# Performance work log

Hardware: AMD Instinct MI355X
Metric: run time of the kernel (lower is better)

Reference implementation:

```python
import jax, jax.numpy as jnp
import numpy as np

N_NODES = 100000
N_EDGES = 1600000
DIM = 64
L = 5
NUM_GRAPHS = 256
BN_EPS = 1e-5


def setup_inputs() -> dict:
    key = jax.random.key(0)
    ks = jax.random.split(key, 8)
    x = jax.random.normal(ks[0], (N_NODES, DIM), dtype=jnp.float32)
    edge_index = jax.random.randint(ks[1], (2, N_EDGES), 0, N_NODES, dtype=jnp.int32).astype(jnp.int64)
    batch = jnp.sort(jax.random.randint(ks[2], (N_NODES,), 0, NUM_GRAPHS, dtype=jnp.int32)).astype(jnp.int64)
    W1 = jax.random.normal(ks[3], (L, DIM, DIM), dtype=jnp.float32) * (1.0 / np.sqrt(DIM))
    b1 = jnp.zeros((L, DIM), dtype=jnp.float32)
    W2 = jax.random.normal(ks[4], (L, DIM, DIM), dtype=jnp.float32) * (1.0 / np.sqrt(DIM))
    b2 = jnp.zeros((L, DIM), dtype=jnp.float32)
    gamma = jnp.ones((L, DIM), dtype=jnp.float32)
    beta = jnp.zeros((L, DIM), dtype=jnp.float32)
    return {"x": x, "edge_index": edge_index, "batch": batch, "W1": W1, "b1": b1, "W2": W2, "b2": b2, "gamma": gamma, "beta": beta}


def reference(x, edge_index, batch, W1, b1, W2, b2, gamma, beta):
    src, dst = edge_index[0], edge_index[1]
    n = x.shape[0]
    h = x
    xs = []
    for i in range(L):
        # GINConv (eps=0): h_i' = MLP(h_i + sum_{j->i} h_j), scatter-add over edges
        agg = jax.ops.segment_sum(h[src], dst, num_segments=n)
        z = h + agg
        z = jnp.maximum(z @ W1[i] + b1[i], 0.0) @ W2[i] + b2[i]
        z = jnp.maximum(z, 0.0)  # outer ReLU
        # BatchNorm1d, training-mode batch stats (biased var)
        mu = jnp.mean(z, axis=0)
        var = jnp.mean((z - mu) ** 2, axis=0)
        z = (z - mu) * jax.lax.rsqrt(var + BN_EPS) * gamma[i] + beta[i]
        xs.append(z)
        h = z
    counts = jax.ops.segment_sum(jnp.ones((n,), dtype=x.dtype), batch, num_segments=NUM_GRAPHS)
    counts = jnp.maximum(counts, 1.0)[:, None]
    xpool = [jax.ops.segment_sum(z, batch, num_segments=NUM_GRAPHS) / counts for z in xs]
    return jnp.concatenate(xpool, axis=1), jnp.concatenate(xs, axis=1)
```

## Files before the change

kernel.cpp:

```cpp
#include <hip/hip_runtime.h>

#define N_NODES 100000
#define N_EDGES 1600000
#define DIM 64
#define NLAYERS 5
#define NUM_GRAPHS 256
#define BN_EPS 1e-5f
#define STATS_BLOCKS 256
#define CSR_CAP 64
#define OV_CAP 65536

__global__ void build_csr_kernel(const int* __restrict__ ei, int* __restrict__ cursor,
                                 int* __restrict__ csr, int* __restrict__ ovcnt,
                                 int* __restrict__ ovedges) {
    int e = blockIdx.x * 256 + threadIdx.x;
    if (e >= N_EDGES) return;
    int s = ei[e];
    int t = ei[N_EDGES + e];
    int slot = atomicAdd(&cursor[t], 1);
    if (slot < CSR_CAP) {
        csr[(long)t * CSR_CAP + slot] = s;
    } else {
        int o = atomicAdd(ovcnt, 1);
        if (o < OV_CAP) ovedges[o] = e;
    }
}

__global__ void pad_csr_kernel(const int* __restrict__ cursor, int* __restrict__ csr) {
    int n = blockIdx.x * 256 + threadIdx.x;
    if (n >= N_NODES) return;
    int cnt = min(cursor[n], CSR_CAP);
    int cnt8 = (cnt + 7) & ~7;
    for (int k = cnt; k < cnt8; ++k) csr[(long)n * CSR_CAP + k] = 0;
}

__global__ __launch_bounds__(256) void aggregate_kernel(
        const int* __restrict__ csr, const int* __restrict__ deg,
        const float* __restrict__ h, int hstride, float* __restrict__ agg) {
    long tid = (long)blockIdx.x * 256 + threadIdx.x;
    int n = (int)(tid >> 6);
    int d = (int)(tid & 63);
    if (n >= N_NODES) return;
    int cnt = min(deg[n], CSR_CAP);
    int cnt8 = (cnt + 7) & ~7;
    const int* row = csr + (long)n * CSR_CAP;
    float a0 = 0.f, a1 = 0.f, a2 = 0.f, a3 = 0.f;
    float a4 = 0.f, a5 = 0.f, a6 = 0.f, a7 = 0.f;
    for (int k = 0; k < cnt8; k += 8) {
        int s0 = row[k + 0], s1 = row[k + 1], s2 = row[k + 2], s3 = row[k + 3];
        int s4 = row[k + 4], s5 = row[k + 5], s6 = row[k + 6], s7 = row[k + 7];
        float v0 = h[(long)s0 * hstride + d];
        float v1 = h[(long)s1 * hstride + d];
        float v2 = h[(long)s2 * hstride + d];
        float v3 = h[(long)s3 * hstride + d];
        float v4 = h[(long)s4 * hstride + d];
        float v5 = h[(long)s5 * hstride + d];
        float v6 = h[(long)s6 * hstride + d];
        float v7 = h[(long)s7 * hstride + d];
        if (k + 0 < cnt) a0 += v0;
        if (k + 1 < cnt) a1 += v1;
        if (k + 2 < cnt) a2 += v2;
        if (k + 3 < cnt) a3 += v3;
        if (k + 4 < cnt) a4 += v4;
        if (k + 5 < cnt) a5 += v5;
        if (k + 6 < cnt) a6 += v6;
        if (k + 7 < cnt) a7 += v7;
    }
    agg[(long)n * DIM + d] = ((a0 + a1) + (a2 + a3)) + ((a4 + a5) + (a6 + a7));
}

__global__ void overflow_kernel(const int* __restrict__ ovedges, const int* __restrict__ ovcnt,
                                const int* __restrict__ ei, const float* __restrict__ h,
                                int hstride, float* __restrict__ agg) {
    int cnt = *ovcnt;
    if (cnt > OV_CAP) cnt = OV_CAP;
    int w = (blockIdx.x * blockDim.x + threadIdx.x) >> 6;
    int d = threadIdx.x & 63;
    int nw = (gridDim.x * blockDim.x) >> 6;
    for (int i = w; i < cnt; i += nw) {
        int e = ovedges[i];
        int s = ei[e];
        int t = ei[N_EDGES + e];
        atomicAdd(&agg[(long)t * DIM + d], h[(long)s * hstride + d]);
    }
}

__global__ __launch_bounds__(256) void mlp_gemm_kernel(
        const float* __restrict__ in, int in_stride, const float* __restrict__ agg,
        const float* __restrict__ W, const float* __restrict__ b,
        float* __restrict__ out) {
    __shared__ __align__(16) float sW[DIM * DIM];
    __shared__ float sb[DIM];
    for (int k = threadIdx.x; k < DIM * DIM / 4; k += 256)
        ((float4*)sW)[k] = ((const float4*)W)[k];
    if (threadIdx.x < DIM) sb[threadIdx.x] = b[threadIdx.x];
    __syncthreads();

    int n = blockIdx.x * 256 + threadIdx.x;
    if (n >= N_NODES) return;
    const float* inr = in + (long)n * in_stride;
    const float* ar = agg ? agg + (long)n * DIM : nullptr;

    float acc[DIM];
#pragma unroll
    for (int j = 0; j < DIM; ++j) acc[j] = sb[j];

    for (int d4 = 0; d4 < DIM / 4; ++d4) {
        float4 zv = *(const float4*)(inr + d4 * 4);
        if (ar) {
            float4 g = *(const float4*)(ar + d4 * 4);
            zv.x += g.x; zv.y += g.y; zv.z += g.z; zv.w += g.w;
        }
        const float* w0 = sW + (d4 * 4 + 0) * DIM;
        const float* w1 = sW + (d4 * 4 + 1) * DIM;
        const float* w2 = sW + (d4 * 4 + 2) * DIM;
        const float* w3 = sW + (d4 * 4 + 3) * DIM;
#pragma unroll
        for (int j = 0; j < DIM; j += 4) {
            float4 a0 = *(const float4*)(w0 + j);
            float4 a1 = *(const float4*)(w1 + j);
            float4 a2 = *(const float4*)(w2 + j);
            float4 a3 = *(const float4*)(w3 + j);
            acc[j + 0] += zv.x * a0.x + zv.y * a1.x + zv.z * a2.x + zv.w * a3.x;
            acc[j + 1] += zv.x * a0.y + zv.y * a1.y + zv.z * a2.y + zv.w * a3.y;
            acc[j + 2] += zv.x * a0.z + zv.y * a1.z + zv.z * a2.z + zv.w * a3.z;
            acc[j + 3] += zv.x * a0.w + zv.y * a1.w + zv.z * a2.w + zv.w * a3.w;
        }
    }

    float* o = out + (long)n * DIM;
#pragma unroll
    for (int k = 0; k < DIM; k += 4) {
        float4 v = { fmaxf(acc[k + 0], 0.f), fmaxf(acc[k + 1], 0.f),
                     fmaxf(acc[k + 2], 0.f), fmaxf(acc[k + 3], 0.f) };
        *(float4*)(o + k) = v;
    }
}

__global__ void stats_partial_kernel(const float* __restrict__ z, float* __restrict__ partials) {
    __shared__ float red[2 * 256];
    int d = threadIdx.x & 63;
    int slot = threadIdx.x >> 6;
    const int S = STATS_BLOCKS * 4;
    float s1 = 0.f, s2 = 0.f;
    int n = blockIdx.x * 4 + slot;
    for (; n + 3 * S < N_NODES; n += 4 * S) {
        float v0 = z[(long)(n + 0 * S) * DIM + d];
        float v1 = z[(long)(n + 1 * S) * DIM + d];
        float v2 = z[(long)(n + 2 * S) * DIM + d];
        float v3 = z[(long)(n + 3 * S) * DIM + d];
        s1 += v0 + v1 + v2 + v3;
        s2 += v0 * v0 + v1 * v1 + v2 * v2 + v3 * v3;
    }
    for (; n < N_NODES; n += S) {
        float v = z[(long)n * DIM + d];
        s1 += v;
        s2 += v * v;
    }
    red[threadIdx.x] = s1;
    red[256 + threadIdx.x] = s2;
    __syncthreads();
    if (threadIdx.x < 64) {
        float a = red[d] + red[64 + d] + red[128 + d] + red[192 + d];
        float c = red[256 + d] + red[320 + d] + red[384 + d] + red[448 + d];
        partials[blockIdx.x * 128 + d] = a;
        partials[blockIdx.x * 128 + 64 + d] = c;
    }
}

__global__ void stats_finalize_kernel(const float* __restrict__ partials,
                                      const float* __restrict__ gamma,
                                      const float* __restrict__ beta,
                                      float* __restrict__ ss) {
    int d = threadIdx.x;
    if (d >= 64) return;
    float s1 = 0.f, s2 = 0.f;
    for (int b = 0; b < STATS_BLOCKS; ++b) {
        s1 += partials[b * 128 + d];
        s2 += partials[b * 128 + 64 + d];
    }
    float mu = s1 * (1.f / N_NODES);
    float var = s2 * (1.f / N_NODES) - mu * mu;
    float rs = 1.f / sqrtf(fmaxf(var, 0.f) + BN_EPS);
    float sc = gamma[d] * rs;
    ss[d] = sc;
    ss[64 + d] = beta[d] - mu * sc;
}

__global__ void bn_apply_kernel(const float* __restrict__ z, const float* __restrict__ ss,
                                float* __restrict__ outxs) {
    long t = (long)blockIdx.x * 256 + threadIdx.x;
    if (t >= (long)N_NODES * (DIM / 4)) return;
    int r = (int)(t & 15);
    long n = t >> 4;
    float4 v = ((const float4*)(z + n * DIM))[r];
    float4 sc = ((const float4*)ss)[r];
    float4 sh = ((const float4*)(ss + DIM))[r];
    float4 o = { v.x * sc.x + sh.x, v.y * sc.y + sh.y,
                 v.z * sc.z + sh.z, v.w * sc.w + sh.w };
    ((float4*)(outxs + n * (DIM * NLAYERS)))[r] = o;
}

__global__ void graph_starts_kernel(const int* __restrict__ batch, int* __restrict__ starts) {
    int g = threadIdx.x;
    if (g > NUM_GRAPHS) return;
    int lo = 0, hi = N_NODES;
    while (lo < hi) {
        int mid = (lo + hi) >> 1;
        if (batch[mid] < g) lo = mid + 1; else hi = mid;
    }
    starts[g] = lo;
}

__global__ void pool_kernel(const float* __restrict__ xs, const int* __restrict__ starts,
                            float* __restrict__ outpool) {
    int g = blockIdx.x;
    int d = threadIdx.x;
    int s = starts[g], e = starts[g + 1];
    const int LD = DIM * NLAYERS;
    float a0 = 0.f, a1 = 0.f, a2 = 0.f, a3 = 0.f;
    float a4 = 0.f, a5 = 0.f, a6 = 0.f, a7 = 0.f;
    int n = s;
    for (; n + 8 <= e; n += 8) {
        a0 += xs[(long)(n + 0) * LD + d];
        a1 += xs[(long)(n + 1) * LD + d];
        a2 += xs[(long)(n + 2) * LD + d];
        a3 += xs[(long)(n + 3) * LD + d];
        a4 += xs[(long)(n + 4) * LD + d];
        a5 += xs[(long)(n + 5) * LD + d];
        a6 += xs[(long)(n + 6) * LD + d];
        a7 += xs[(long)(n + 7) * LD + d];
    }
    for (; n < e; ++n) a0 += xs[(long)n * LD + d];
    float acc = ((a0 + a1) + (a2 + a3)) + ((a4 + a5) + (a6 + a7));
    outpool[(long)g * LD + d] = acc / fmaxf((float)(e - s), 1.f);
}

static inline size_t rup(size_t x) { return (x + 255) & ~(size_t)255; }

extern "C" void kernel_launch(void* const* d_in, const int* in_sizes, int n_in,
                              void* d_out, int out_size, void* d_ws, size_t ws_size,
                              hipStream_t stream) {
    const float* x     = (const float*)d_in[0];
    const int*   ei    = (const int*)d_in[1];
    const int*   batch = (const int*)d_in[2];
    const float* W1    = (const float*)d_in[3];
    const float* b1    = (const float*)d_in[4];
    const float* W2    = (const float*)d_in[5];
    const float* b2    = (const float*)d_in[6];
    const float* gamma = (const float*)d_in[7];
    const float* beta  = (const float*)d_in[8];

    float* out      = (float*)d_out;
    float* out_pool = out;
    float* out_xs   = out + (size_t)NUM_GRAPHS * DIM * NLAYERS;

    char* w = (char*)d_ws;
    int*   csr      = (int*)w;    w += rup((size_t)N_NODES * CSR_CAP * 4);
    int*   cursor   = (int*)w;    w += rup((size_t)N_NODES * 4);
    int*   ovcnt    = (int*)w;    w += 256;
    int*   ovedges  = (int*)w;    w += rup((size_t)OV_CAP * 4);
    float* agg      = (float*)w;  w += rup((size_t)N_NODES * DIM * 4);
    float* bufB     = (float*)w;  w += rup((size_t)N_NODES * DIM * 4);
    float* partials = (float*)w;  w += rup((size_t)STATS_BLOCKS * 128 * 4);
    float* ss       = (float*)w;  w += 512;
    int*   starts   = (int*)w;    w += rup((size_t)(NUM_GRAPHS + 1) * 4);

    hipMemsetAsync(cursor, 0, (size_t)N_NODES * 4, stream);
    hipMemsetAsync(ovcnt, 0, 4, stream);
    build_csr_kernel<<<(N_EDGES + 255) / 256, 256, 0, stream>>>(ei, cursor, csr, ovcnt, ovedges);
    pad_csr_kernel<<<(N_NODES + 255) / 256, 256, 0, stream>>>(cursor, csr);
    graph_starts_kernel<<<1, 320, 0, stream>>>(batch, starts);

    const float* h = x;
    int hs = DIM;
    for (int l = 0; l < NLAYERS; ++l) {
        aggregate_kernel<<<((long)N_NODES * DIM + 255) / 256, 256, 0, stream>>>(csr, cursor, h, hs, agg);
        overflow_kernel<<<16, 256, 0, stream>>>(ovedges, ovcnt, ei, h, hs, agg);
        mlp_gemm_kernel<<<(N_NODES + 255) / 256, 256, 0, stream>>>(
            h, hs, agg, W1 + (size_t)l * DIM * DIM, b1 + (size_t)l * DIM, bufB);
        mlp_gemm_kernel<<<(N_NODES + 255) / 256, 256, 0, stream>>>(
            bufB, DIM, nullptr, W2 + (size_t)l * DIM * DIM, b2 + (size_t)l * DIM, agg);
        stats_partial_kernel<<<STATS_BLOCKS, 256, 0, stream>>>(agg, partials);
        stats_finalize_kernel<<<1, 64, 0, stream>>>(partials, gamma + (size_t)l * DIM,
                                                    beta + (size_t)l * DIM, ss);
        bn_apply_kernel<<<((long)N_NODES * (DIM / 4) + 255) / 256, 256, 0, stream>>>(
            agg, ss, out_xs + (size_t)l * DIM);
        h = out_xs + (size_t)l * DIM;
        hs = DIM * NLAYERS;
    }

    pool_kernel<<<NUM_GRAPHS, 320, 0, stream>>>(out_xs, starts, out_pool);
}
```

Measured before the change: 966.6 us.

## Fuse two MLP GEMMs with BN stats, shrink CSR cap, inline overflow handling

Merges the two per-layer MLP GEMM kernels and the BatchNorm partial-statistics pass into one kernel that keeps the hidden activations in registers and reduces per-block sums via wave shuffles. This removes the intermediate buffer round trip and two launches per layer. The CSR row capacity is halved to cut index memory and padding. Overflow edges are now stored as (dst,src) pairs and scanned linearly inside the aggregate kernel, which replaces the atomic overflow kernel but could be costly if many nodes exceed the smaller cap. CSR building also processes four edges per thread. Register pressure in the fused MLP (two 64-float accumulators) may reduce occupancy.

After: 1.795 ms. 85.7% more time.

```diff
diff --git a/kernel.cpp b/kernel.cpp
--- a/kernel.cpp
+++ b/kernel.cpp
@@ -6,24 +6,32 @@
 #define NLAYERS 5
 #define NUM_GRAPHS 256
 #define BN_EPS 1e-5f
-#define STATS_BLOCKS 256
-#define CSR_CAP 64
+#define CSR_CAP 32
 #define OV_CAP 65536
-
-__global__ void build_csr_kernel(const int* __restrict__ ei, int* __restrict__ cursor,
-                                 int* __restrict__ csr, int* __restrict__ ovcnt,
-                                 int* __restrict__ ovedges) {
-    int e = blockIdx.x * 256 + threadIdx.x;
-    if (e >= N_EDGES) return;
-    int s = ei[e];
-    int t = ei[N_EDGES + e];
-    int slot = atomicAdd(&cursor[t], 1);
-    if (slot < CSR_CAP) {
-        csr[(long)t * CSR_CAP + slot] = s;
-    } else {
-        int o = atomicAdd(ovcnt, 1);
-        if (o < OV_CAP) ovedges[o] = e;
-    }
+#define NBLK ((N_NODES + 255) / 256)
+
+__global__ __launch_bounds__(256) void build_csr_kernel(
+        const int* __restrict__ ei, int* __restrict__ cursor,
+        int* __restrict__ csr, int* __restrict__ ovcnt, int* __restrict__ ovpairs) {
+    const int Q = N_EDGES / 4;
+    int tid = blockIdx.x * 256 + threadIdx.x;
+    if (tid >= Q) return;
+    int e0 = tid, e1 = tid + Q, e2 = tid + 2 * Q, e3 = tid + 3 * Q;
+    int s0 = ei[e0], s1 = ei[e1], s2 = ei[e2], s3 = ei[e3];
+    int t0 = ei[N_EDGES + e0], t1 = ei[N_EDGES + e1];
+    int t2 = ei[N_EDGES + e2], t3 = ei[N_EDGES + e3];
+    int c0 = atomicAdd(&cursor[t0], 1);
+    int c1 = atomicAdd(&cursor[t1], 1);
+    int c2 = atomicAdd(&cursor[t2], 1);
+    int c3 = atomicAdd(&cursor[t3], 1);
+    if (c0 < CSR_CAP) csr[t0 * CSR_CAP + c0] = s0;
+    else { int o = atomicAdd(ovcnt, 1); if (o < OV_CAP) { ovpairs[2*o] = t0; ovpairs[2*o+1] = s0; } }
+    if (c1 < CSR_CAP) csr[t1 * CSR_CAP + c1] = s1;
+    else { int o = atomicAdd(ovcnt, 1); if (o < OV_CAP) { ovpairs[2*o] = t1; ovpairs[2*o+1] = s1; } }
+    if (c2 < CSR_CAP) csr[t2 * CSR_CAP + c2] = s2;
+    else { int o = atomicAdd(ovcnt, 1); if (o < OV_CAP) { ovpairs[2*o] = t2; ovpairs[2*o+1] = s2; } }
+    if (c3 < CSR_CAP) csr[t3 * CSR_CAP + c3] = s3;
+    else { int o = atomicAdd(ovcnt, 1); if (o < OV_CAP) { ovpairs[2*o] = t3; ovpairs[2*o+1] = s3; } }
 }
 
 __global__ void pad_csr_kernel(const int* __restrict__ cursor, int* __restrict__ csr) {
@@ -31,32 +39,34 @@
     if (n >= N_NODES) return;
     int cnt = min(cursor[n], CSR_CAP);
     int cnt8 = (cnt + 7) & ~7;
-    for (int k = cnt; k < cnt8; ++k) csr[(long)n * CSR_CAP + k] = 0;
+    for (int k = cnt; k < cnt8; ++k) csr[n * CSR_CAP + k] = 0;
 }
 
 __global__ __launch_bounds__(256) void aggregate_kernel(
         const int* __restrict__ csr, const int* __restrict__ deg,
+        const int* __restrict__ ovcnt, const int* __restrict__ ovpairs,
         const float* __restrict__ h, int hstride, float* __restrict__ agg) {
     long tid = (long)blockIdx.x * 256 + threadIdx.x;
     int n = (int)(tid >> 6);
     int d = (int)(tid & 63);
     if (n >= N_NODES) return;
-    int cnt = min(deg[n], CSR_CAP);
+    int dval = deg[n];
+    int cnt = min(dval, CSR_CAP);
     int cnt8 = (cnt + 7) & ~7;
-    const int* row = csr + (long)n * CSR_CAP;
+    const int4* row = (const int4*)(csr + n * CSR_CAP);
     float a0 = 0.f, a1 = 0.f, a2 = 0.f, a3 = 0.f;
     float a4 = 0.f, a5 = 0.f, a6 = 0.f, a7 = 0.f;
     for (int k = 0; k < cnt8; k += 8) {
-        int s0 = row[k + 0], s1 = row[k + 1], s2 = row[k + 2], s3 = row[k + 3];
-        int s4 = row[k + 4], s5 = row[k + 5], s6 = row[k + 6], s7 = row[k + 7];
-        float v0 = h[(long)s0 * hstride + d];
-        float v1 = h[(long)s1 * hstride + d];
-        float v2 = h[(long)s2 * hstride + d];
-        float v3 = h[(long)s3 * hstride + d];
-        float v4 = h[(long)s4 * hstride + d];
-        float v5 = h[(long)s5 * hstride + d];
-        float v6 = h[(long)s6 * hstride + d];
-        float v7 = h[(long)s7 * hstride + d];
+        int4 ra = row[k >> 2];
+        int4 rb = row[(k >> 2) + 1];
+        float v0 = h[(long)ra.x * hstride + d];
+        float v1 = h[(long)ra.y * hstride + d];
+        float v2 = h[(long)ra.z * hstride + d];
+        float v3 = h[(long)ra.w * hstride + d];
+        float v4 = h[(long)rb.x * hstride + d];
+        float v5 = h[(long)rb.y * hstride + d];
+        float v6 = h[(long)rb.z * hstride + d];
+        float v7 = h[(long)rb.w * hstride + d];
         if (k + 0 < cnt) a0 += v0;
         if (k + 1 < cnt) a1 += v1;
         if (k + 2 < cnt) a2 += v2;
@@ -66,105 +76,121 @@
         if (k + 6 < cnt) a6 += v6;
         if (k + 7 < cnt) a7 += v7;
     }
+    if (dval > CSR_CAP) {
+        int m = min(*ovcnt, OV_CAP);
+        for (int i = 0; i < m; ++i) {
+            if (ovpairs[2 * i] == n) a0 += h[(long)ovpairs[2 * i + 1] * hstride + d];
+        }
+    }
     agg[(long)n * DIM + d] = ((a0 + a1) + (a2 + a3)) + ((a4 + a5) + (a6 + a7));
 }
 
-__global__ void overflow_kernel(const int* __restrict__ ovedges, const int* __restrict__ ovcnt,
-                                const int* __restrict__ ei, const float* __restrict__ h,
-                                int hstride, float* __restrict__ agg) {
-    int cnt = *ovcnt;
-    if (cnt > OV_CAP) cnt = OV_CAP;
-    int w = (blockIdx.x * blockDim.x + threadIdx.x) >> 6;
-    int d = threadIdx.x & 63;
-    int nw = (gridDim.x * blockDim.x) >> 6;
-    for (int i = w; i < cnt; i += nw) {
-        int e = ovedges[i];
-        int s = ei[e];
-        int t = ei[N_EDGES + e];
-        atomicAdd(&agg[(long)t * DIM + d], h[(long)s * hstride + d]);
-    }
-}
-
-__global__ __launch_bounds__(256) void mlp_gemm_kernel(
+__global__ __launch_bounds__(256) void mlp_fused_kernel(
         const float* __restrict__ in, int in_stride, const float* __restrict__ agg,
-        const float* __restrict__ W, const float* __restrict__ b,
-        float* __restrict__ out) {
-    __shared__ __align__(16) float sW[DIM * DIM];
-    __shared__ float sb[DIM];
-    for (int k = threadIdx.x; k < DIM * DIM / 4; k += 256)
-        ((float4*)sW)[k] = ((const float4*)W)[k];
-    if (threadIdx.x < DIM) sb[threadIdx.x] = b[threadIdx.x];
+        const float* __restrict__ W1, const float* __restrict__ b1,
+        const float* __restrict__ W2, const float* __restrict__ b2,
+        float* __restrict__ z, float* __restrict__ partials) {
+    __shared__ __align__(16) float sW1[DIM * DIM];
+    __shared__ __align__(16) float sW2[DIM * DIM];
+    __shared__ float sb1[DIM], sb2[DIM];
+    __shared__ float red[4][2][DIM];
+    for (int k = threadIdx.x; k < DIM * DIM / 4; k += 256) {
+        ((float4*)sW1)[k] = ((const float4*)W1)[k];
+        ((float4*)sW2)[k] = ((const float4*)W2)[k];
+    }
+    if (threadIdx.x < DIM) { sb1[threadIdx.x] = b1[threadIdx.x]; sb2[threadIdx.x] = b2[threadIdx.x]; }
     __syncthreads();
 
     int n = blockIdx.x * 256 + threadIdx.x;
-    if (n >= N_NODES) return;
-    const float* inr = in + (long)n * in_stride;
-    const float* ar = agg ? agg + (long)n * DIM : nullptr;
-
-    float acc[DIM];
-#pragma unroll
-    for (int j = 0; j < DIM; ++j) acc[j] = sb[j];
-
-    for (int d4 = 0; d4 < DIM / 4; ++d4) {
-        float4 zv = *(const float4*)(inr + d4 * 4);
-        if (ar) {
-            float4 g = *(const float4*)(ar + d4 * 4);
+    bool valid = n < N_NODES;
+
+    float acc1[DIM];
+    float acc2[DIM];
+#pragma unroll
+    for (int j = 0; j < DIM; ++j) acc1[j] = sb1[j];
+#pragma unroll
+    for (int j = 0; j < DIM; ++j) acc2[j] = valid ? sb2[j] : 0.f;
+
+    if (valid) {
+        const float* inr = in + (long)n * in_stride;
+        const float* ar  = agg + (long)n * DIM;
+        for (int d4 = 0; d4 < DIM / 4; ++d4) {
+            float4 zv = ((const float4*)inr)[d4];
+            float4 g  = ((const float4*)ar)[d4];
             zv.x += g.x; zv.y += g.y; zv.z += g.z; zv.w += g.w;
-        }
-        const float* w0 = sW + (d4 * 4 + 0) * DIM;
-        const float* w1 = sW + (d4 * 4 + 1) * DIM;
-        const float* w2 = sW + (d4 * 4 + 2) * DIM;
-        const float* w3 = sW + (d4 * 4 + 3) * DIM;
+            const float* w0 = sW1 + (d4 * 4 + 0) * DIM;
+            const float* w1 = sW1 + (d4 * 4 + 1) * DIM;
+            const float* w2 = sW1 + (d4 * 4 + 2) * DIM;
+            const float* w3 = sW1 + (d4 * 4 + 3) * DIM;
+#pragma unroll
+            for (int j = 0; j < DIM; j += 4) {
+                float4 a0 = *(const float4*)(w0 + j);
+                float4 a1 = *(const float4*)(w1 + j);
+                float4 a2 = *(const float4*)(w2 + j);
+                float4 a3 = *(const float4*)(w3 + j);
+                acc1[j + 0] += zv.x * a0.x + zv.y * a1.x + zv.z * a2.x + zv.w * a3.x;
+                acc1[j + 1] += zv.x * a0.y + zv.y * a1.y + zv.z * a2.y + zv.w * a3.y;
+                acc1[j + 2] += zv.x * a0.z + zv.y * a1.z + zv.z * a2.z + zv.w * a3.z;
+                acc1[j + 3] += zv.x * a0.w + zv.y * a1.w + zv.z * a2.w + zv.w * a3.w;
+            }
+        }
+#pragma unroll
+        for (int k4 = 0; k4 < DIM / 4; ++k4) {
+            float h0 = fmaxf(acc1[4 * k4 + 0], 0.f);
+            float h1 = fmaxf(acc1[4 * k4 + 1], 0.f);
+            float h2 = fmaxf(acc1[4 * k4 + 2], 0.f);
+            float h3 = fmaxf(acc1[4 * k4 + 3], 0.f);
+            const float* w0 = sW2 + (4 * k4 + 0) * DIM;
+            const float* w1 = sW2 + (4 * k4 + 1) * DIM;
+            const float* w2 = sW2 + (4 * k4 + 2) * DIM;
+            const float* w3 = sW2 + (4 * k4 + 3) * DIM;
+#pragma unroll
+            for (int j = 0; j < DIM; j += 4) {
+                float4 a0 = *(const float4*)(w0 + j);
+                float4 a1 = *(const float4*)(w1 + j);
+                float4 a2 = *(const float4*)(w2 + j);
+                float4 a3 = *(const float4*)(w3 + j);
+                acc2[j + 0] += h0 * a0.x + h1 * a1.x + h2 * a2.x + h3 * a3.x;
+                acc2[j + 1] += h0 * a0.y + h1 * a1.y + h2 * a2.y + h3 * a3.y;
+                acc2[j + 2] += h0 * a0.z + h1 * a1.z + h2 * a2.z + h3 * a3.z;
+                acc2[j + 3] += h0 * a0.w + h1 * a1.w + h2 * a2.w + h3 * a3.w;
+            }
+        }
+    }
+
+#pragma unroll
+    for (int j = 0; j < DIM; ++j) acc2[j] = fmaxf(acc2[j], 0.f);
+    if (valid) {
+        float* o = z + (long)n * DIM;
 #pragma unroll
         for (int j = 0; j < DIM; j += 4) {
-            float4 a0 = *(const float4*)(w0 + j);
-            float4 a1 = *(const float4*)(w1 + j);
-            float4 a2 = *(const float4*)(w2 + j);
-            float4 a3 = *(const float4*)(w3 + j);
-            acc[j + 0] += zv.x * a0.x + zv.y * a1.x + zv.z * a2.x + zv.w * a3.x;
-            acc[j + 1] += zv.x * a0.y + zv.y * a1.y + zv.z * a2.y + zv.w * a3.y;
-            acc[j + 2] += zv.x * a0.z + zv.y * a1.z + zv.z * a2.z + zv.w * a3.z;
-            acc[j + 3] += zv.x * a0.w + zv.y * a1.w + zv.z * a2.w + zv.w * a3.w;
-        }
-    }
-
-    float* o = out + (long)n * DIM;
-#pragma unroll
-    for (int k = 0; k < DIM; k += 4) {
-        float4 v = { fmaxf(acc[k + 0], 0.f), fmaxf(acc[k + 1], 0.f),
-                     fmaxf(acc[k + 2], 0.f), fmaxf(acc[k + 3], 0.f) };
-        *(float4*)(o + k) = v;
-    }
-}
-
-__global__ void stats_partial_kernel(const float* __restrict__ z, float* __restrict__ partials) {
-    __shared__ float red[2 * 256];
-    int d = threadIdx.x & 63;
-    int slot = threadIdx.x >> 6;
-    const int S = STATS_BLOCKS * 4;
-    float s1 = 0.f, s2 = 0.f;
-    int n = blockIdx.x * 4 + slot;
-    for (; n + 3 * S < N_NODES; n += 4 * S) {
-        float v0 = z[(long)(n + 0 * S) * DIM + d];
-        float v1 = z[(long)(n + 1 * S) * DIM + d];
-        float v2 = z[(long)(n + 2 * S) * DIM + d];
-        float v3 = z[(long)(n + 3 * S) * DIM + d];
-        s1 += v0 + v1 + v2 + v3;
-        s2 += v0 * v0 + v1 * v1 + v2 * v2 + v3 * v3;
-    }
-    for (; n < N_NODES; n += S) {
-        float v = z[(long)n * DIM + d];
-        s1 += v;
-        s2 += v * v;
-    }
-    red[threadIdx.x] = s1;
-    red[256 + threadIdx.x] = s2;
+            float4 v = { acc2[j], acc2[j + 1], acc2[j + 2], acc2[j + 3] };
+            *(float4*)(o + j) = v;
+        }
+    }
+
+    int lane = threadIdx.x & 63;
+    int wv = threadIdx.x >> 6;
+    float p1 = 0.f, p2 = 0.f;
+#pragma unroll
+    for (int j = 0; j < DIM; ++j) {
+        float v1 = acc2[j];
+        float v2 = v1 * v1;
+#pragma unroll
+        for (int s = 1; s < 64; s <<= 1) {
+            v1 += __shfl_xor(v1, s, 64);
+            v2 += __shfl_xor(v2, s, 64);
+        }
+        if (lane == j) { p1 = v1; p2 = v2; }
+    }
+    red[wv][0][lane] = p1;
+    red[wv][1][lane] = p2;
     __syncthreads();
-    if (threadIdx.x < 64) {
-        float a = red[d] + red[64 + d] + red[128 + d] + red[192 + d];
-        float c = red[256 + d] + red[320 + d] + red[384 + d] + red[448 + d];
-        partials[blockIdx.x * 128 + d] = a;
-        partials[blockIdx.x * 128 + 64 + d] = c;
+    if (threadIdx.x < 128) {
+        int which = threadIdx.x >> 6;
+        int dd = threadIdx.x & 63;
+        float s = red[0][which][dd] + red[1][which][dd] + red[2][which][dd] + red[3][which][dd];
+        partials[blockIdx.x * 128 + which * 64 + dd] = s;
     }
 }
 
@@ -172,19 +198,26 @@
                                       const float* __restrict__ gamma,
                                       const float* __restrict__ beta,
                                       float* __restrict__ ss) {
-    int d = threadIdx.x;
-    if (d >= 64) return;
+    __shared__ float r1[256], r2[256];
+    int d = threadIdx.x & 63, q = threadIdx.x >> 6;
     float s1 = 0.f, s2 = 0.f;
-    for (int b = 0; b < STATS_BLOCKS; ++b) {
+    for (int b = q; b < NBLK; b += 4) {
         s1 += partials[b * 128 + d];
         s2 += partials[b * 128 + 64 + d];
     }
-    float mu = s1 * (1.f / N_NODES);
-    float var = s2 * (1.f / N_NODES) - mu * mu;
-    float rs = 1.f / sqrtf(fmaxf(var, 0.f) + BN_EPS);
-    float sc = gamma[d] * rs;
-    ss[d] = sc;
-    ss[64 + d] = beta[d] - mu * sc;
+    r1[threadIdx.x] = s1;
+    r2[threadIdx.x] = s2;
+    __syncthreads();
+    if (threadIdx.x < 64) {
+        s1 = r1[d] + r1[64 + d] + r1[128 + d] + r1[192 + d];
+        s2 = r2[d] + r2[64 + d] + r2[128 + d] + r2[192 + d];
+        float mu = s1 * (1.f / N_NODES);
+        float var = s2 * (1.f / N_NODES) - mu * mu;
+        float rs = 1.f / sqrtf(fmaxf(var, 0.f) + BN_EPS);
+        float sc = gamma[d] * rs;
+        ss[d] = sc;
+        ss[64 + d] = beta[d] - mu * sc;
+    }
 }
 
 __global__ void bn_apply_kernel(const float* __restrict__ z, const float* __restrict__ ss,
@@ -259,33 +292,33 @@
     int*   csr      = (int*)w;    w += rup((size_t)N_NODES * CSR_CAP * 4);
     int*   cursor   = (int*)w;    w += rup((size_t)N_NODES * 4);
     int*   ovcnt    = (int*)w;    w += 256;
-    int*   ovedges  = (int*)w;    w += rup((size_t)OV_CAP * 4);
+    int*   ovpairs  = (int*)w;    w += rup((size_t)OV_CAP * 8);
     float* agg      = (float*)w;  w += rup((size_t)N_NODES * DIM * 4);
     float* bufB     = (float*)w;  w += rup((size_t)N_NODES * DIM * 4);
-    float* partials = (float*)w;  w += rup((size_t)STATS_BLOCKS * 128 * 4);
+    float* partials = (float*)w;  w += rup((size_t)NBLK * 128 * 4);
     float* ss       = (float*)w;  w += 512;
     int*   starts   = (int*)w;    w += rup((size_t)(NUM_GRAPHS + 1) * 4);
 
     hipMemsetAsync(cursor, 0, (size_t)N_NODES * 4, stream);
     hipMemsetAsync(ovcnt, 0, 4, stream);
-    build_csr_kernel<<<(N_EDGES + 255) / 256, 256, 0, stream>>>(ei, cursor, csr, ovcnt, ovedges);
-    pad_csr_kernel<<<(N_NODES + 255) / 256, 256, 0, stream>>>(cursor, csr);
+    build_csr_kernel<<<(N_EDGES / 4 + 255) / 256, 256, 0, stream>>>(ei, cursor, csr, ovcnt, ovpairs);
+    pad_csr_kernel<<<NBLK, 256, 0, stream>>>(cursor, csr);
     graph_starts_kernel<<<1, 320, 0, stream>>>(batch, starts);
 
     const float* h = x;
     int hs = DIM;
     for (int l = 0; l < NLAYERS; ++l) {
-        aggregate_kernel<<<((long)N_NODES * DIM + 255) / 256, 256, 0, stream>>>(csr, cursor, h, hs, agg);
-        overflow_kernel<<<16, 256, 0, stream>>>(ovedges, ovcnt, ei, h, hs, agg);
-        mlp_gemm_kernel<<<(N_NODES + 255) / 256, 256, 0, stream>>>(
-            h, hs, agg, W1 + (size_t)l * DIM * DIM, b1 + (size_t)l * DIM, bufB);
-        mlp_gemm_kernel<<<(N_NODES + 255) / 256, 256, 0, stream>>>(
-            bufB, DIM, nullptr, W2 + (size_t)l * DIM * DIM, b2 + (size_t)l * DIM, agg);
-        stats_partial_kernel<<<STATS_BLOCKS, 256, 0, stream>>>(agg, partials);
-        stats_finalize_kernel<<<1, 64, 0, stream>>>(partials, gamma + (size_t)l * DIM,
-                                                    beta + (size_t)l * DIM, ss);
+        aggregate_kernel<<<((long)N_NODES * DIM + 255) / 256, 256, 0, stream>>>(
+            csr, cursor, ovcnt, ovpairs, h, hs, agg);
+        mlp_fused_kernel<<<NBLK, 256, 0, stream>>>(
+            h, hs, agg,
+            W1 + (size_t)l * DIM * DIM, b1 + (size_t)l * DIM,
+            W2 + (size_t)l * DIM * DIM, b2 + (size_t)l * DIM,
+            bufB, partials);
+        stats_finalize_kernel<<<1, 256, 0, stream>>>(partials, gamma + (size_t)l * DIM,
+                                                     beta + (size_t)l * DIM, ss);
         bn_apply_kernel<<<((long)N_NODES * (DIM / 4) + 255) / 256, 256, 0, stream>>>(
-            agg, ss, out_xs + (size_t)l * DIM);
+            bufB, ss, out_xs + (size_t)l * DIM);
         h = out_xs + (size_t)l * DIM;
         hs = DIM * NLAYERS;
     }
```
